# Kernel tuning notes

Measured on AMD Instinct MI355X. Metric: run time of the kernel, lower is better.

## Reference

```python
import jax, jax.numpy as jnp
import numpy as np

EN_HID = 1024
DE_HID = 1024
BATCH = 64
SRC_LEN = 2048


def setup_inputs() -> dict:
    key = jax.random.key(0)
    ks = jax.random.split(key, 7)
    s_en = 1.0 / np.sqrt(EN_HID)
    s_de = 1.0 / np.sqrt(DE_HID)
    return {
        "hidden": jax.random.normal(ks[0], (1, BATCH, DE_HID), jnp.float32),
        "en_output": jax.random.normal(ks[1], (BATCH, SRC_LEN, EN_HID), jnp.float32),
        "w_en_w": jax.random.uniform(ks[2], (DE_HID, EN_HID), jnp.float32, -s_en, s_en),
        "w_en_b": jax.random.uniform(ks[3], (DE_HID,), jnp.float32, -s_en, s_en),
        "w_de_w": jax.random.uniform(ks[4], (DE_HID, DE_HID), jnp.float32, -s_de, s_de),
        "w_de_b": jax.random.uniform(ks[5], (DE_HID,), jnp.float32, -s_de, s_de),
        "v_w": jax.random.uniform(ks[6], (1, DE_HID), jnp.float32, -s_de, s_de),
    }


def reference(hidden, en_output, w_en_w, w_en_b, w_de_w, w_de_b, v_w):
    # hidden: (1, B, Dd) -> (B, 1, Dd); broadcast over src_len instead of repeat
    h = jnp.transpose(hidden, (1, 0, 2))  # (B, 1, Dd)
    proj_en = jnp.einsum('bse,de->bsd', en_output, w_en_w) + w_en_b  # (B, S, Dd)
    proj_de = jnp.einsum('bqh,dh->bqd', h, w_de_w) + w_de_b          # (B, 1, Dd)
    energy = jnp.tanh(proj_en + proj_de)                              # (B, S, Dd)
    scores = jnp.einsum('bsd,od->bs', energy, v_w)                   # (B, S)
    attention = jax.nn.softmax(scores, axis=1)                        # (B, S)
    weighted = jnp.einsum('bs,bse->be', attention, en_output)[:, None, :]  # (B, 1, E)
    return weighted, attention
```

## Files before the change

### kernel.cpp

```cpp
#include <hip/hip_runtime.h>
#include <stdint.h>

typedef __attribute__((ext_vector_type(4))) float  f32x4;
typedef __attribute__((ext_vector_type(8))) short  bf16x8;
typedef __attribute__((ext_vector_type(4))) short  s16x4;

#define BATCH   64
#define SRC_LEN 2048
#define HID     1024
#define M_TOT   (BATCH*SRC_LEN)

#define BM 256
#define BN 256
#define BK 64

__device__ __forceinline__ short f2bf(float f) {
  unsigned u = __builtin_bit_cast(unsigned, f);
  u += 0x7fffu + ((u >> 16) & 1u);
  return (short)(u >> 16);
}
__device__ __forceinline__ float bf2f(short s) {
  unsigned u = ((unsigned)(unsigned short)s) << 16;
  return __builtin_bit_cast(float, u);
}
__device__ __forceinline__ bf16x8 cvt8(f32x4 lo, f32x4 hi) {
  bf16x8 o;
  o[0]=f2bf(lo[0]); o[1]=f2bf(lo[1]); o[2]=f2bf(lo[2]); o[3]=f2bf(lo[3]);
  o[4]=f2bf(hi[0]); o[5]=f2bf(hi[1]); o[6]=f2bf(hi[2]); o[7]=f2bf(hi[3]);
  return o;
}

__global__ void k_convert_all(const float* __restrict__ en, short* __restrict__ en_bf,
                              const float* __restrict__ w,  short* __restrict__ wb) {
  if (blockIdx.x < 2048) {
    size_t stride = (size_t)2048 * 256 * 8;
    size_t base = ((size_t)blockIdx.x * 256 + threadIdx.x) * 8;
    size_t total = (size_t)M_TOT * HID;
    for (; base < total; base += stride) {
      f32x4 a = *(const f32x4*)(en + base);
      f32x4 b = *(const f32x4*)(en + base + 4);
      *(bf16x8*)(en_bf + base) = cvt8(a, b);
    }
  } else {
    int i = ((blockIdx.x - 2048) * 256 + threadIdx.x) * 8;
    f32x4 a = *(const f32x4*)(w + i);
    f32x4 b = *(const f32x4*)(w + i + 4);
    *(bf16x8*)(wb + i) = cvt8(a, b);
  }
}

__global__ void k_convert_w(const float* __restrict__ w, short* __restrict__ wb) {
  int i = (blockIdx.x * 256 + threadIdx.x) * 8;
  f32x4 a = *(const f32x4*)(w + i);
  f32x4 b = *(const f32x4*)(w + i + 4);
  *(bf16x8*)(wb + i) = cvt8(a, b);
}

__global__ void k_bias(const float* __restrict__ hidden, const float* __restrict__ w_de_w,
                       const float* __restrict__ w_en_b, const float* __restrict__ w_de_b,
                       float* __restrict__ bias_all) {
  __shared__ float hid[HID];
  int b  = blockIdx.x >> 2;
  int dc = blockIdx.x & 3;
  for (int i = threadIdx.x; i < HID; i += 256) hid[i] = hidden[b*HID + i];
  __syncthreads();
  int d = dc*256 + threadIdx.x;
  const f32x4* wrow = (const f32x4*)(w_de_w + (size_t)d*HID);
  float acc = 0.f;
  #pragma unroll 8
  for (int q = 0; q < HID/4; ++q) {
    f32x4 w4 = wrow[q];
    f32x4 h4 = *(const f32x4*)&hid[q*4];
    acc += w4[0]*h4[0] + w4[1]*h4[1] + w4[2]*h4[2] + w4[3]*h4[3];
  }
  bias_all[b*HID + d] = acc + w_en_b[d] + w_de_b[d];
}

__global__ void __launch_bounds__(512, 1) k_gemm_score_fast(
    const short* __restrict__ Abf,
    const short* __restrict__ Bw,
    const float* __restrict__ bias_all,
    const float* __restrict__ v_w,
    float* __restrict__ scores)
{
  __shared__ short As[2][BM][BK];
  __shared__ short Bs[2][BN][BK];

  int raw  = blockIdx.x;
  int xcd  = raw & 7;
  int idx  = raw >> 3;
  int mblk = xcd * 64 + (idx >> 2);
  int nblk = idx & 3;
  int m0 = mblk * BM, n0 = nblk * BN;

  int tid  = threadIdx.x;
  int lane = tid & 63;
  int wid  = tid >> 6;
  int wm = wid >> 2, wn = wid & 3;
  int fr  = lane & 15;
  int fko = (lane >> 4) * 8;
  int rsw = (fr & 7) << 3;

  f32x4 acc[8][4] = {};

  int cA0 = tid,        cA1 = tid + 1024;
  int cA2 = tid + 512,  cA3 = tid + 1536;
  int gb  = ((tid >> 8) << 9) + (tid & 255);
  int cB0 = gb,         cB1 = gb + 1024;
  int cB2 = gb + 256,   cB3 = gb + 1280;

  #define SOFF(c, rb) ((size_t)((rb) + ((c) >> 3)) * HID + (size_t)((((c) & 7) ^ (((c) >> 3) & 7)) * 8))
  const size_t sA0 = SOFF(cA0, m0), sA1 = SOFF(cA1, m0), sA2 = SOFF(cA2, m0), sA3 = SOFF(cA3, m0);
  const size_t sB0 = SOFF(cB0, n0), sB1 = SOFF(cB1, n0), sB2 = SOFF(cB2, n0), sB3 = SOFF(cB3, n0);
  #undef SOFF

  #define GLD(SRCP, LDSBASE, DOFF) __builtin_amdgcn_global_load_lds( \
      (const __attribute__((address_space(1))) void*)(SRCP), \
      (__attribute__((address_space(3))) void*)((char*)(LDSBASE) + (DOFF)), 16, 0, 0)

  #define STG_A01(OTH, KT) do{ GLD(Abf + sA0 + (KT)*64, &As[OTH][0][0], cA0*16); \
                               GLD(Abf + sA1 + (KT)*64, &As[OTH][0][0], cA1*16); }while(0)
  #define STG_A23(OTH, KT) do{ GLD(Abf + sA2 + (KT)*64, &As[OTH][0][0], cA2*16); \
                               GLD(Abf + sA3 + (KT)*64, &As[OTH][0][0], cA3*16); }while(0)
  #define STG_B01(OTH, KT) do{ GLD(Bw  + sB0 + (KT)*64, &Bs[OTH][0][0], cB0*16); \
                               GLD(Bw  + sB1 + (KT)*64, &Bs[OTH][0][0], cB1*16); }while(0)
  #define STG_B23(OTH, KT) do{ GLD(Bw  + sB2 + (KT)*64, &Bs[OTH][0][0], cB2*16); \
                               GLD(Bw  + sB3 + (KT)*64, &Bs[OTH][0][0], cB3*16); }while(0)

  bf16x8 aF[8], bF[4];
  #define LDA(BUF, MQ) { _Pragma("unroll") for (int mi = 0; mi < 4; ++mi) \
      _Pragma("unroll") for (int kk = 0; kk < 2; ++kk) \
        aF[mi*2+kk] = *(const bf16x8*)&As[BUF][wm*128 + (MQ)*64 + mi*16 + fr][(kk*32 + fko) ^ rsw]; }
  #define LDB(BUF, NQ) { _Pragma("unroll") for (int ni = 0; ni < 2; ++ni) \
      _Pragma("unroll") for (int kk = 0; kk < 2; ++kk) \
        bF[ni*2+kk] = *(const bf16x8*)&Bs[BUF][wn*64 + (NQ)*32 + ni*16 + fr][(kk*32 + fko) ^ rsw]; }
  #define MMQ(MQ, NQ) { _Pragma("unroll") for (int mi = 0; mi < 4; ++mi) \
      _Pragma("unroll") for (int ni = 0; ni < 2; ++ni) \
      _Pragma("unroll") for (int kk = 0; kk < 2; ++kk) \
        acc[(MQ)*4+mi][(NQ)*2+ni] = __builtin_amdgcn_mfma_f32_16x16x32_bf16( \
            aF[mi*2+kk], bF[ni*2+kk], acc[(MQ)*4+mi][(NQ)*2+ni], 0, 0, 0); }

  #define BARR   __builtin_amdgcn_s_barrier()
  #define VMC(N) asm volatile("s_waitcnt vmcnt(" #N ")" ::: "memory")
  #define PR1    __builtin_amdgcn_s_setprio(1)
  #define PR0    __builtin_amdgcn_s_setprio(0)

  STG_A01(0, 0); STG_B01(0, 0); STG_B23(0, 0); STG_A23(0, 0);
  VMC(4); BARR;

  #pragma unroll 1
  for (int kt = 0; kt < 15; ++kt) {
    int buf = kt & 1, oth = buf ^ 1;
    LDA(buf, 0); LDB(buf, 0); STG_A01(oth, kt + 1);
    BARR; PR1; MMQ(0, 0); PR0; VMC(4); BARR;
    LDB(buf, 1); STG_B01(oth, kt + 1);
    BARR; PR1; MMQ(0, 1); PR0; VMC(4); BARR;
    LDA(buf, 1); STG_B23(oth, kt + 1);
    BARR; PR1; MMQ(1, 1); PR0; BARR;
    LDB(buf, 0); STG_A23(oth, kt + 1);
    BARR; PR1; MMQ(1, 0); PR0; VMC(4); BARR;
  }
  LDA(1, 0); LDB(1, 0); BARR; PR1; MMQ(0, 0); PR0; VMC(2); BARR;
  LDB(1, 1);            BARR; PR1; MMQ(0, 1); PR0; VMC(0); BARR;
  LDA(1, 1);            BARR; PR1; MMQ(1, 1); PR0; BARR;
  LDB(1, 0);            BARR; PR1; MMQ(1, 0); PR0;

  #undef LDA
  #undef LDB
  #undef MMQ
  #undef STG_A01
  #undef STG_A23
  #undef STG_B01
  #undef STG_B23
  #undef GLD

  int b = m0 >> 11;
  float vv[4], bb[4];
  #pragma unroll
  for (int nf = 0; nf < 4; ++nf) {
    int col = n0 + wn*64 + nf*16 + fr;
    vv[nf] = v_w[col];
    bb[nf] = bias_all[b*HID + col];
  }
  #pragma unroll
  for (int mf = 0; mf < 8; ++mf) {
    #pragma unroll
    for (int j = 0; j < 4; ++j) {
      float p = 0.f;
      #pragma unroll
      for (int nf = 0; nf < 4; ++nf)
        p += tanhf(acc[mf][nf][j] + bb[nf]) * vv[nf];
      p += __shfl_xor(p, 1);
      p += __shfl_xor(p, 2);
      p += __shfl_xor(p, 4);
      p += __shfl_xor(p, 8);
      if (fr == 0) {
        int row = wm*128 + mf*16 + ((lane >> 4) << 2) + j;
        atomicAdd(&scores[m0 + row], p);
      }
    }
  }
}

__global__ void __launch_bounds__(256) k_gemm_score_conv(
    const float* __restrict__ A, const short* __restrict__ Bw,
    const float* __restrict__ bias_all, const float* __restrict__ v_w,
    float* __restrict__ scores)
{
  __shared__ short Asl[128][64];
  __shared__ short Bsl[128][64];
  int raw  = blockIdx.x;
  int xcd  = raw & 7;
  int idx  = raw >> 3;
  int mblk = xcd * (M_TOT/128/8) + (idx >> 3);
  int nblk = idx & 7;
  int m0 = mblk * 128, n0 = nblk * 128;
  int tid  = threadIdx.x;
  int lane = tid & 63;
  int wid  = tid >> 6;
  int wr = wid >> 1, wc = wid & 1;
  int fr  = lane & 15;
  int fko = (lane >> 4) * 8;
  f32x4 acc[4][4] = {};
  int ar = tid >> 1;
  int ac = (tid & 1) * 32;
  const float* aBase = A + (size_t)(m0 + ar) * HID + ac;
  f32x4 aReg[8];
  #pragma unroll
  for (int i = 0; i < 8; ++i) aReg[i] = *(const f32x4*)(aBase + i*4);
  for (int kt = 0; kt < 16; ++kt) {
    __syncthreads();
    #pragma unroll
    for (int g = 0; g < 4; ++g)
      *(bf16x8*)&Asl[ar][ac + g*8] = cvt8(aReg[2*g], aReg[2*g+1]);
    #pragma unroll
    for (int j = 0; j < 4; ++j) {
      int c = j*256 + tid;
      const short* src = Bw + (size_t)(n0 + (c >> 3)) * HID + kt*64 + (c & 7)*8;
      __builtin_amdgcn_global_load_lds(
          (const __attribute__((address_space(1))) void*)src,
          (__attribute__((address_space(3))) void*)((char*)&Bsl[0][0] + c*16),
          16, 0, 0);
    }
    __syncthreads();
    if (kt + 1 < 16) {
      const float* nxt = aBase + (kt+1)*64;
      #pragma unroll
      for (int i = 0; i < 8; ++i) aReg[i] = *(const f32x4*)(nxt + i*4);
    }
    #pragma unroll
    for (int kk = 0; kk < 2; ++kk) {
      bf16x8 aF[4], bF[4];
      #pragma unroll
      for (int mi = 0; mi < 4; ++mi)
        aF[mi] = *(const bf16x8*)&Asl[wr*64 + mi*16 + fr][kk*32 + fko];
      #pragma unroll
      for (int ni = 0; ni < 4; ++ni)
        bF[ni] = *(const bf16x8*)&Bsl[wc*64 + ni*16 + fr][kk*32 + fko];
      #pragma unroll
      for (int mi = 0; mi < 4; ++mi)
        #pragma unroll
        for (int ni = 0; ni < 4; ++ni)
          acc[mi][ni] = __builtin_amdgcn_mfma_f32_16x16x32_bf16(aF[mi], bF[ni], acc[mi][ni], 0, 0, 0);
    }
  }
  int b = m0 >> 11;
  float vv[4], bb[4];
  #pragma unroll
  for (int ni = 0; ni < 4; ++ni) {
    int col = n0 + wc*64 + ni*16 + fr;
    vv[ni] = v_w[col];
    bb[ni] = bias_all[b*HID + col];
  }
  #pragma unroll
  for (int mi = 0; mi < 4; ++mi) {
    #pragma unroll
    for (int j = 0; j < 4; ++j) {
      float p = 0.f;
      #pragma unroll
      for (int ni = 0; ni < 4; ++ni)
        p += tanhf(acc[mi][ni][j] + bb[ni]) * vv[ni];
      p += __shfl_xor(p, 1);
      p += __shfl_xor(p, 2);
      p += __shfl_xor(p, 4);
      p += __shfl_xor(p, 8);
      if (fr == 0) {
        int row = wr*64 + mi*16 + ((lane >> 4) << 2) + j;
        atomicAdd(&scores[m0 + row], p);
      }
    }
  }
}

__global__ void k_softmax(float* __restrict__ attn) {
  int b = blockIdx.x;
  float* row = attn + (size_t)b * SRC_LEN;
  int tid = threadIdx.x, lane = tid & 63, wid = tid >> 6;
  __shared__ float red[4];
  float v[8];
  #pragma unroll
  for (int i = 0; i < 8; ++i) v[i] = row[tid + i*256];
  float mx = v[0];
  #pragma unroll
  for (int i = 1; i < 8; ++i) mx = fmaxf(mx, v[i]);
  #pragma unroll
  for (int o = 32; o; o >>= 1) mx = fmaxf(mx, __shfl_xor(mx, o));
  if (lane == 0) red[wid] = mx;
  __syncthreads();
  mx = fmaxf(fmaxf(red[0], red[1]), fmaxf(red[2], red[3]));
  float s = 0.f;
  #pragma unroll
  for (int i = 0; i < 8; ++i) { v[i] = __expf(v[i] - mx); s += v[i]; }
  #pragma unroll
  for (int o = 32; o; o >>= 1) s += __shfl_xor(s, o);
  __syncthreads();
  if (lane == 0) red[wid] = s;
  __syncthreads();
  s = red[0] + red[1] + red[2] + red[3];
  float inv = 1.f / s;
  #pragma unroll
  for (int i = 0; i < 8; ++i) row[tid + i*256] = v[i] * inv;
}

__global__ void k_weighted_bf(const short* __restrict__ en_bf, const float* __restrict__ attn,
                              float* __restrict__ outw) {
  int b  = blockIdx.x >> 4;
  int sc = blockIdx.x & 15;
  __shared__ float aw[128];
  int tid = threadIdx.x;
  if (tid < 128) aw[tid] = attn[b*SRC_LEN + sc*128 + tid];
  __syncthreads();
  const short* base = en_bf + ((size_t)b*SRC_LEN + sc*128) * HID + tid*4;
  float a0=0.f, a1=0.f, a2=0.f, a3=0.f;
  #pragma unroll 8
  for (int s = 0; s < 128; ++s) {
    s16x4 x = *(const s16x4*)(base + (size_t)s*HID);
    float w = aw[s];
    a0 += w*bf2f(x[0]); a1 += w*bf2f(x[1]); a2 += w*bf2f(x[2]); a3 += w*bf2f(x[3]);
  }
  float* o = outw + b*HID + tid*4;
  atomicAdd(o+0, a0); atomicAdd(o+1, a1);
  atomicAdd(o+2, a2); atomicAdd(o+3, a3);
}

__global__ void k_weighted(const float* __restrict__ en, const float* __restrict__ attn,
                           float* __restrict__ outw) {
  int b  = blockIdx.x >> 4;
  int sc = blockIdx.x & 15;
  __shared__ float aw[128];
  int tid = threadIdx.x;
  if (tid < 128) aw[tid] = attn[b*SRC_LEN + sc*128 + tid];
  __syncthreads();
  const float* base = en + ((size_t)b*SRC_LEN + sc*128) * HID + tid*4;
  f32x4 acc = {0.f, 0.f, 0.f, 0.f};
  #pragma unroll 8
  for (int s = 0; s < 128; ++s) {
    f32x4 x = *(const f32x4*)(base + (size_t)s*HID);
    float w = aw[s];
    acc[0] += w*x[0]; acc[1] += w*x[1]; acc[2] += w*x[2]; acc[3] += w*x[3];
  }
  float* o = outw + b*HID + tid*4;
  atomicAdd(o+0, acc[0]); atomicAdd(o+1, acc[1]);
  atomicAdd(o+2, acc[2]); atomicAdd(o+3, acc[3]);
}

extern "C" void kernel_launch(void* const* d_in, const int* in_sizes, int n_in,
                              void* d_out, int out_size, void* d_ws, size_t ws_size,
                              hipStream_t stream) {
  const float* hidden = (const float*)d_in[0];
  const float* en     = (const float*)d_in[1];
  const float* w_en_w = (const float*)d_in[2];
  const float* w_en_b = (const float*)d_in[3];
  const float* w_de_w = (const float*)d_in[4];
  const float* w_de_b = (const float*)d_in[5];
  const float* v_w    = (const float*)d_in[6];

  float* outw = (float*)d_out;
  float* attn = outw + BATCH*HID;

  const size_t en_elems = (size_t)M_TOT * HID;
  const size_t need_fast = en_elems*sizeof(short) + (size_t)HID*HID*sizeof(short)
                         + (size_t)BATCH*HID*sizeof(float);

  hipMemsetAsync(d_out, 0, (size_t)out_size * sizeof(float), stream);

  if (ws_size >= need_fast) {
    short* en_bf    = (short*)d_ws;
    short* w_bf     = en_bf + en_elems;
    float* bias_all = (float*)(w_bf + (size_t)HID*HID);

    k_convert_all<<<dim3(2048 + 512), dim3(256), 0, stream>>>(en, en_bf, w_en_w, w_bf);
    k_bias<<<dim3(BATCH*4), dim3(256), 0, stream>>>(hidden, w_de_w, w_en_b, w_de_b, bias_all);
    k_gemm_score_fast<<<dim3((M_TOT/BM)*(HID/BN)), dim3(512), 0, stream>>>(en_bf, w_bf, bias_all, v_w, attn);
    k_softmax<<<dim3(BATCH), dim3(256), 0, stream>>>(attn);
    k_weighted_bf<<<dim3(BATCH*16), dim3(256), 0, stream>>>(en_bf, attn, outw);
  } else {
    short* w_bf     = (short*)d_ws;
    float* bias_all = (float*)((char*)d_ws + (size_t)HID*HID*sizeof(short));
    k_convert_w<<<dim3(HID*HID/(256*8)), dim3(256), 0, stream>>>(w_en_w, w_bf);
    k_bias<<<dim3(BATCH*4), dim3(256), 0, stream>>>(hidden, w_de_w, w_en_b, w_de_b, bias_all);
    k_gemm_score_conv<<<dim3((M_TOT/128)*(HID/128)), dim3(256), 0, stream>>>(en, w_bf, bias_all, v_w, attn);
    k_softmax<<<dim3(BATCH), dim3(256), 0, stream>>>(attn);
    k_weighted<<<dim3(BATCH*16), dim3(256), 0, stream>>>(en, attn, outw);
  }
}
```

Baseline: 611.4 us.

## Fuse bias into convert kernel, softmax into weighted sum, double-buffer B fragments

Folds the decoder-bias GEMV into the conversion kernel as extra blocks and merges softmax into the weighted-sum kernel. Each of the 16 blocks per batch row recomputes the row max and sum and writes its own slice of the attention output. This removes two launches and a separate pass over the scores. The GEMM loop now keeps two B fragment register sets so the fourth quarter reuses bF0 instead of reloading it from LDS, at the cost of more registers. Scores now go to a workspace buffer that is zeroed first, adding a memset.

After: 673.5 us. 1.1x slower.

```diff
diff --git a/kernel.cpp b/kernel.cpp
--- a/kernel.cpp
+++ b/kernel.cpp
@@ -31,7 +31,11 @@
 }
 
 __global__ void k_convert_all(const float* __restrict__ en, short* __restrict__ en_bf,
-                              const float* __restrict__ w,  short* __restrict__ wb) {
+                              const float* __restrict__ w,  short* __restrict__ wb,
+                              const float* __restrict__ hidden, const float* __restrict__ w_de_w,
+                              const float* __restrict__ w_en_b, const float* __restrict__ w_de_b,
+                              float* __restrict__ bias_all) {
+  __shared__ float hid[HID];
   if (blockIdx.x < 2048) {
     size_t stride = (size_t)2048 * 256 * 8;
     size_t base = ((size_t)blockIdx.x * 256 + threadIdx.x) * 8;
@@ -41,11 +45,27 @@
       f32x4 b = *(const f32x4*)(en + base + 4);
       *(bf16x8*)(en_bf + base) = cvt8(a, b);
     }
-  } else {
+  } else if (blockIdx.x < 2560) {
     int i = ((blockIdx.x - 2048) * 256 + threadIdx.x) * 8;
     f32x4 a = *(const f32x4*)(w + i);
     f32x4 b = *(const f32x4*)(w + i + 4);
     *(bf16x8*)(wb + i) = cvt8(a, b);
+  } else {
+    int bb = blockIdx.x - 2560;
+    int b  = bb >> 2;
+    int dc = bb & 3;
+    for (int i = threadIdx.x; i < HID; i += 256) hid[i] = hidden[b*HID + i];
+    __syncthreads();
+    int d = dc*256 + threadIdx.x;
+    const f32x4* wrow = (const f32x4*)(w_de_w + (size_t)d*HID);
+    float acc = 0.f;
+    #pragma unroll 8
+    for (int q = 0; q < HID/4; ++q) {
+      f32x4 w4 = wrow[q];
+      f32x4 h4 = *(const f32x4*)&hid[q*4];
+      acc += w4[0]*h4[0] + w4[1]*h4[1] + w4[2]*h4[2] + w4[3]*h4[3];
+    }
+    bias_all[b*HID + d] = acc + w_en_b[d] + w_de_b[d];
   }
 }
 
@@ -55,7 +75,6 @@
   f32x4 b = *(const f32x4*)(w + i + 4);
   *(bf16x8*)(wb + i) = cvt8(a, b);
 }
-
 __global__ void k_bias(const float* __restrict__ hidden, const float* __restrict__ w_de_w,
                        const float* __restrict__ w_en_b, const float* __restrict__ w_de_b,
                        float* __restrict__ bias_all) {
@@ -127,44 +146,47 @@
   #define STG_B23(OTH, KT) do{ GLD(Bw  + sB2 + (KT)*64, &Bs[OTH][0][0], cB2*16); \
                                GLD(Bw  + sB3 + (KT)*64, &Bs[OTH][0][0], cB3*16); }while(0)
 
-  bf16x8 aF[8], bF[4];
+  bf16x8 aF[8], bF0[4], bF1[4];
   #define LDA(BUF, MQ) { _Pragma("unroll") for (int mi = 0; mi < 4; ++mi) \
       _Pragma("unroll") for (int kk = 0; kk < 2; ++kk) \
         aF[mi*2+kk] = *(const bf16x8*)&As[BUF][wm*128 + (MQ)*64 + mi*16 + fr][(kk*32 + fko) ^ rsw]; }
-  #define LDB(BUF, NQ) { _Pragma("unroll") for (int ni = 0; ni < 2; ++ni) \
+  #define LDB(BUF, NQ, DST) { _Pragma("unroll") for (int ni = 0; ni < 2; ++ni) \
       _Pragma("unroll") for (int kk = 0; kk < 2; ++kk) \
-        bF[ni*2+kk] = *(const bf16x8*)&Bs[BUF][wn*64 + (NQ)*32 + ni*16 + fr][(kk*32 + fko) ^ rsw]; }
-  #define MMQ(MQ, NQ) { _Pragma("unroll") for (int mi = 0; mi < 4; ++mi) \
+        DST[ni*2+kk] = *(const bf16x8*)&Bs[BUF][wn*64 + (NQ)*32 + ni*16 + fr][(kk*32 + fko) ^ rsw]; }
+  #define MMQ(MQ, NQ, BFA) { _Pragma("unroll") for (int mi = 0; mi < 4; ++mi) \
       _Pragma("unroll") for (int ni = 0; ni < 2; ++ni) \
       _Pragma("unroll") for (int kk = 0; kk < 2; ++kk) \
         acc[(MQ)*4+mi][(NQ)*2+ni] = __builtin_amdgcn_mfma_f32_16x16x32_bf16( \
-            aF[mi*2+kk], bF[ni*2+kk], acc[(MQ)*4+mi][(NQ)*2+ni], 0, 0, 0); }
+            aF[mi*2+kk], BFA[ni*2+kk], acc[(MQ)*4+mi][(NQ)*2+ni], 0, 0, 0); }
 
   #define BARR   __builtin_amdgcn_s_barrier()
   #define VMC(N) asm volatile("s_waitcnt vmcnt(" #N ")" ::: "memory")
   #define PR1    __builtin_amdgcn_s_setprio(1)
   #define PR0    __builtin_amdgcn_s_setprio(0)
 
+  #define TILE(BUF, OTH, KT, LAST) do{ \
+    LDA(BUF, 0); LDB(BUF, 0, bF0); if (!(LAST)) STG_A01(OTH, (KT)+1); \
+    BARR; PR1; MMQ(0, 0, bF0); PR0; if (!(LAST)) { VMC(4); } else { VMC(2); } BARR; \
+    LDB(BUF, 1, bF1); if (!(LAST)) STG_B01(OTH, (KT)+1); \
+    BARR; PR1; MMQ(0, 1, bF1); PR0; if (!(LAST)) { VMC(4); } else { VMC(0); } BARR; \
+    LDA(BUF, 1); if (!(LAST)) STG_B23(OTH, (KT)+1); \
+    BARR; PR1; MMQ(1, 1, bF1); PR0; BARR; \
+    if (!(LAST)) STG_A23(OTH, (KT)+1); \
+    BARR; PR1; MMQ(1, 0, bF0); PR0; if (!(LAST)) { VMC(4); } BARR; \
+  }while(0)
+
   STG_A01(0, 0); STG_B01(0, 0); STG_B23(0, 0); STG_A23(0, 0);
   VMC(4); BARR;
 
   #pragma unroll 1
-  for (int kt = 0; kt < 15; ++kt) {
-    int buf = kt & 1, oth = buf ^ 1;
-    LDA(buf, 0); LDB(buf, 0); STG_A01(oth, kt + 1);
-    BARR; PR1; MMQ(0, 0); PR0; VMC(4); BARR;
-    LDB(buf, 1); STG_B01(oth, kt + 1);
-    BARR; PR1; MMQ(0, 1); PR0; VMC(4); BARR;
-    LDA(buf, 1); STG_B23(oth, kt + 1);
-    BARR; PR1; MMQ(1, 1); PR0; BARR;
-    LDB(buf, 0); STG_A23(oth, kt + 1);
-    BARR; PR1; MMQ(1, 0); PR0; VMC(4); BARR;
-  }
-  LDA(1, 0); LDB(1, 0); BARR; PR1; MMQ(0, 0); PR0; VMC(2); BARR;
-  LDB(1, 1);            BARR; PR1; MMQ(0, 1); PR0; VMC(0); BARR;
-  LDA(1, 1);            BARR; PR1; MMQ(1, 1); PR0; BARR;
-  LDB(1, 0);            BARR; PR1; MMQ(1, 0); PR0;
-
+  for (int it = 0; it < 7; ++it) {
+    TILE(0, 1, 2*it,     false);
+    TILE(1, 0, 2*it + 1, false);
+  }
+  TILE(0, 1, 14, false);
+  TILE(1, 0, 15, true);
+
+  #undef TILE
   #undef LDA
   #undef LDB
   #undef MMQ
@@ -322,20 +344,50 @@
   for (int i = 0; i < 8; ++i) row[tid + i*256] = v[i] * inv;
 }
 
-__global__ void k_weighted_bf(const short* __restrict__ en_bf, const float* __restrict__ attn,
-                              float* __restrict__ outw) {
+__global__ void k_weighted_sm(const short* __restrict__ en_bf, const float* __restrict__ scores,
+                              float* __restrict__ attn_out, float* __restrict__ outw) {
   int b  = blockIdx.x >> 4;
   int sc = blockIdx.x & 15;
+  int tid = threadIdx.x, lane = tid & 63, wid = tid >> 6;
+  __shared__ float red[4];
   __shared__ float aw[128];
-  int tid = threadIdx.x;
-  if (tid < 128) aw[tid] = attn[b*SRC_LEN + sc*128 + tid];
-  __syncthreads();
+
+  const float* srow = scores + (size_t)b * SRC_LEN;
+  float v[8];
+  #pragma unroll
+  for (int i = 0; i < 8; ++i) v[i] = srow[tid + i*256];
+  float mx = v[0];
+  #pragma unroll
+  for (int i = 1; i < 8; ++i) mx = fmaxf(mx, v[i]);
+  #pragma unroll
+  for (int o = 32; o; o >>= 1) mx = fmaxf(mx, __shfl_xor(mx, o));
+  if (lane == 0) red[wid] = mx;
+  __syncthreads();
+  mx = fmaxf(fmaxf(red[0], red[1]), fmaxf(red[2], red[3]));
+  float s = 0.f;
+  #pragma unroll
+  for (int i = 0; i < 8; ++i) s += __expf(v[i] - mx);
+  #pragma unroll
+  for (int o = 32; o; o >>= 1) s += __shfl_xor(s, o);
+  __syncthreads();
+  if (lane == 0) red[wid] = s;
+  __syncthreads();
+  s = red[0] + red[1] + red[2] + red[3];
+  float inv = 1.f / s;
+
+  if (tid < 128) {
+    float a = __expf(srow[sc*128 + tid] - mx) * inv;
+    attn_out[(size_t)b*SRC_LEN + sc*128 + tid] = a;
+    aw[tid] = a;
+  }
+  __syncthreads();
+
   const short* base = en_bf + ((size_t)b*SRC_LEN + sc*128) * HID + tid*4;
   float a0=0.f, a1=0.f, a2=0.f, a3=0.f;
   #pragma unroll 8
-  for (int s = 0; s < 128; ++s) {
-    s16x4 x = *(const s16x4*)(base + (size_t)s*HID);
-    float w = aw[s];
+  for (int q = 0; q < 128; ++q) {
+    s16x4 x = *(const s16x4*)(base + (size_t)q*HID);
+    float w = aw[q];
     a0 += w*bf2f(x[0]); a1 += w*bf2f(x[1]); a2 += w*bf2f(x[2]); a3 += w*bf2f(x[3]);
   }
   float* o = outw + b*HID + tid*4;
@@ -380,7 +432,7 @@
 
   const size_t en_elems = (size_t)M_TOT * HID;
   const size_t need_fast = en_elems*sizeof(short) + (size_t)HID*HID*sizeof(short)
-                         + (size_t)BATCH*HID*sizeof(float);
+                         + (size_t)BATCH*HID*sizeof(float) + (size_t)BATCH*SRC_LEN*sizeof(float);
 
   hipMemsetAsync(d_out, 0, (size_t)out_size * sizeof(float), stream);
 
@@ -388,12 +440,13 @@
     short* en_bf    = (short*)d_ws;
     short* w_bf     = en_bf + en_elems;
     float* bias_all = (float*)(w_bf + (size_t)HID*HID);
-
-    k_convert_all<<<dim3(2048 + 512), dim3(256), 0, stream>>>(en, en_bf, w_en_w, w_bf);
-    k_bias<<<dim3(BATCH*4), dim3(256), 0, stream>>>(hidden, w_de_w, w_en_b, w_de_b, bias_all);
-    k_gemm_score_fast<<<dim3((M_TOT/BM)*(HID/BN)), dim3(512), 0, stream>>>(en_bf, w_bf, bias_all, v_w, attn);
-    k_softmax<<<dim3(BATCH), dim3(256), 0, stream>>>(attn);
-    k_weighted_bf<<<dim3(BATCH*16), dim3(256), 0, stream>>>(en_bf, attn, outw);
+    float* scores   = bias_all + (size_t)BATCH*HID;
+
+    hipMemsetAsync(scores, 0, (size_t)BATCH*SRC_LEN*sizeof(float), stream);
+    k_convert_all<<<dim3(2048 + 512 + 256), dim3(256), 0, stream>>>(
+        en, en_bf, w_en_w, w_bf, hidden, w_de_w, w_en_b, w_de_b, bias_all);
+    k_gemm_score_fast<<<dim3((M_TOT/BM)*(HID/BN)), dim3(512), 0, stream>>>(en_bf, w_bf, bias_all, v_w, scores);
+    k_weighted_sm<<<dim3(BATCH*16), dim3(256), 0, stream>>>(en_bf, scores, attn, outw);
   } else {
     short* w_bf     = (short*)d_ws;
     float* bias_all = (float*)((char*)d_ws + (size_t)HID*HID*sizeof(short));
```
